# Optimization experiments

Measured on AMD Instinct MI355X. Metric: run time of the kernel, lower is better.

Reference implementation:

```python
import jax, jax.numpy as jnp
import numpy as np
from jax import lax

INF = jnp.float32(1e30)  # large finite stand-in for np.inf (keeps vjp NaN-free)


def setup_inputs() -> dict:
    key = jax.random.key(0)
    k1, k2 = jax.random.split(key)
    M = 2048
    N = 2048
    source = jax.random.normal(k1, (M,), dtype=jnp.float32)
    target = jax.random.normal(k2, (N,), dtype=jnp.float32)
    return {"source": source, "target": target}


def _dtw_sq(source, target):
    # DP over rows: row i holds DTW[i, 0..n]. Only two rows live at a time.
    n = target.shape[0]
    row0 = jnp.concatenate([jnp.zeros((1,), jnp.float32),
                            jnp.full((n,), INF, jnp.float32)])  # DTW[0, :]

    def row_step(prev_row, s_i):
        dists = (s_i - target) ** 2  # [n], cost of cell (i, j)

        def cell(left, xs):
            d, up_left, up = xs  # DTW[i-1,j-1], DTW[i-1,j]; left = DTW[i,j-1]
            cur = d + jnp.minimum(jnp.minimum(up, left), up_left)
            return cur, cur

        _, row_vals = lax.scan(cell, INF, (dists, prev_row[:-1], prev_row[1:]))
        new_row = jnp.concatenate([jnp.full((1,), INF, jnp.float32), row_vals])
        return new_row, None

    final_row, _ = lax.scan(row_step, row0, source)
    return final_row[-1]  # DTW[m, n]


def reference(source, target):
    loss_sq = _dtw_sq(source, target)
    return jnp.sqrt(loss_sq)[None]  # shape (1,), matching torch.Tensor([..])
```

## Files before the change

kernel.cpp:

```cpp
#include <hip/hip_runtime.h>
#include <math.h>


#define MM 2048
#define NN 2048
#define BR 8
#define BC 8
#define NT 256
#define NB (MM / BR)
#define NPH (NB + NT - 1)
#define EXW 9
#define SW 9
#define INFV 1e30f

__launch_bounds__(NT, 1)
__global__ void dtw_kernel(const float* __restrict__ src,
                           const float* __restrict__ tgt,
                           float* __restrict__ out)
{
    __shared__ float s_pad[NB * SW];
    __shared__ float ex[2][NT * EXW];

    const int tid = threadIdx.x;

    for (int i = tid; i < MM; i += NT)
        s_pad[(i >> 3) * SW + (i & 7)] = src[i];

    float tg[BC];
    #pragma unroll
    for (int k = 0; k < BC; ++k) tg[k] = tgt[tid * BC + k];

    float cur[BC];
    #pragma unroll
    for (int k = 0; k < BC; ++k) cur[k] = INFV;

    float corner = (tid == 0) ? 0.0f : INFV;

    __syncthreads();

    for (int p = 0; p < NPH; ++p) {
        const int bi = p - tid;
        if (0 <= bi && bi < NB) {
            float lc[BR];
            if (tid > 0) {
                const float* e = &ex[(p + 1) & 1][(tid - 1) * EXW];
                #pragma unroll
                for (int r = 0; r < BR; ++r) lc[r] = e[r];
            } else {
                #pragma unroll
                for (int r = 0; r < BR; ++r) lc[r] = INFV;
            }
            const float* sp = &s_pad[bi * SW];
            float srow[BR];
            #pragma unroll
            for (int r = 0; r < BR; ++r) srow[r] = sp[r];

            float rc[BR];
            float dl = corner;
            #pragma unroll
            for (int r = 0; r < BR; ++r) {
                float l  = lc[r];
                float sv = srow[r];
                float dgk = dl;
                #pragma unroll
                for (int k = 0; k < BC; ++k) {
                    float up = cur[k];
                    float m  = fminf(fminf(up, l), dgk);
                    float d  = sv - tg[k];
                    float v  = fmaf(d, d, m);
                    dgk = up;
                    cur[k] = v;
                    l = v;
                }
                rc[r] = l;
                dl = lc[r];
            }
            corner = lc[BR - 1];

            float* w = &ex[p & 1][tid * EXW];
            #pragma unroll
            for (int r = 0; r < BR; ++r) w[r] = rc[r];
        }
        __syncthreads();
    }

    if (tid == NT - 1)
        out[0] = sqrtf(cur[BC - 1]);
}

extern "C" void kernel_launch(void* const* d_in, const int* in_sizes, int n_in,
                              void* d_out, int out_size, void* d_ws, size_t ws_size,
                              hipStream_t stream)
{
    (void)in_sizes; (void)n_in; (void)out_size; (void)d_ws; (void)ws_size;
    const float* source = (const float*)d_in[0];
    const float* target = (const float*)d_in[1];
    float* out = (float*)d_out;
    dtw_kernel<<<1, NT, 0, stream>>>(source, target, out);
}
```

Measured before the change: 280.6 us.

## Pass DTW boundaries via wavefront shuffles and skewed mailboxes, sync every KK steps

Replaces the per-diagonal block-wide barrier and shared-memory boundary exchange with intra-wavefront __shfl_up for neighbour column values. Cross-wavefront boundaries go through a ring-buffer mailbox, and each wave is skewed by DELTA steps so it only needs a __syncthreads every KK iterations. The row tile drops to 4 and the cell updates are reordered into an anti-diagonal sweep to expose ILP. The cost is extra pipeline fill/drain from the skew and a total iteration count that grows to NB plus the maximum skew.

```diff
diff --git a/kernel.cpp b/kernel.cpp
--- a/kernel.cpp
+++ b/kernel.cpp
@@ -4,13 +4,16 @@
 
 #define MM 2048
 #define NN 2048
-#define BR 8
+#define BR 4
 #define BC 8
 #define NT 256
 #define NB (MM / BR)
-#define NPH (NB + NT - 1)
-#define EXW 9
-#define SW 9
+#define KK 16
+#define DELTA (63 + KK)
+#define MAXSKEW (63 + 3 * DELTA)
+#define NITER (NB + MAXSKEW)
+#define NSP ((NITER + KK - 1) / KK)
+#define RING (2 * KK)
 #define INFV 1e30f
 
 __launch_bounds__(NT, 1)
@@ -18,13 +21,16 @@
                            const float* __restrict__ tgt,
                            float* __restrict__ out)
 {
-    __shared__ float s_pad[NB * SW];
-    __shared__ float ex[2][NT * EXW];
+    __shared__ float4 s_src4[NB];
+    __shared__ float4 mbox[3][RING];
 
-    const int tid = threadIdx.x;
+    const int tid  = threadIdx.x;
+    const int wv   = tid >> 6;
+    const int ln   = tid & 63;
+    const int skew = ln + wv * DELTA;
 
-    for (int i = tid; i < MM; i += NT)
-        s_pad[(i >> 3) * SW + (i & 7)] = src[i];
+    const float4* s4 = (const float4*)src;
+    for (int i = tid; i < NB; i += NT) s_src4[i] = s4[i];
 
     float tg[BC];
     #pragma unroll
@@ -35,57 +41,67 @@
     for (int k = 0; k < BC; ++k) cur[k] = INFV;
 
     float corner = (tid == 0) ? 0.0f : INFV;
+    float4 rcp = make_float4(INFV, INFV, INFV, INFV);
 
     __syncthreads();
 
-    for (int p = 0; p < NPH; ++p) {
-        const int bi = p - tid;
-        if (0 <= bi && bi < NB) {
-            float lc[BR];
-            if (tid > 0) {
-                const float* e = &ex[(p + 1) & 1][(tid - 1) * EXW];
+    for (int sp = 0; sp < NSP; ++sp) {
+        #pragma unroll 1
+        for (int it = 0; it < KK; ++it) {
+            const int n = sp * KK + it;
+
+            float lc0 = __shfl_up(rcp.x, 1);
+            float lc1 = __shfl_up(rcp.y, 1);
+            float lc2 = __shfl_up(rcp.z, 1);
+            float lc3 = __shfl_up(rcp.w, 1);
+            if (ln == 0) {
+                if (wv == 0) {
+                    lc0 = lc1 = lc2 = lc3 = INFV;
+                } else {
+                    float4 m = mbox[wv - 1][(n - KK) & (RING - 1)];
+                    lc0 = m.x; lc1 = m.y; lc2 = m.z; lc3 = m.w;
+                }
+            }
+
+            const int bi = n - skew;
+            if (0 <= bi && bi < NB) {
+                float4 sv = s_src4[bi];
+                float srow[BR] = {sv.x, sv.y, sv.z, sv.w};
+                float lcx[BR]  = {lc0, lc1, lc2, lc3};
+
+                float dg[BR], lv[BR];
+                dg[0] = corner;
+                lv[0] = lcx[0];
                 #pragma unroll
-                for (int r = 0; r < BR; ++r) lc[r] = e[r];
-            } else {
+                for (int r = 1; r < BR; ++r) { dg[r] = lcx[r - 1]; lv[r] = lcx[r]; }
+
                 #pragma unroll
-                for (int r = 0; r < BR; ++r) lc[r] = INFV;
+                for (int s = 0; s < BR + BC - 1; ++s) {
+                    #pragma unroll
+                    for (int r = 0; r < BR; ++r) {
+                        const int k = s - r;
+                        if (0 <= k && k < BC) {
+                            float up = cur[k];
+                            float m  = fminf(fminf(up, lv[r]), dg[r]);
+                            float d  = srow[r] - tg[k];
+                            float v  = fmaf(d, d, m);
+                            dg[r] = up;
+                            lv[r] = v;
+                            cur[k] = v;
+                        }
+                    }
+                }
+
+                corner = lcx[BR - 1];
+                rcp = make_float4(lv[0], lv[1], lv[2], lv[3]);
+                if (ln == 63 && wv < 3)
+                    mbox[wv][n & (RING - 1)] = rcp;
             }
-            const float* sp = &s_pad[bi * SW];
-            float srow[BR];
-            #pragma unroll
-            for (int r = 0; r < BR; ++r) srow[r] = sp[r];
-
-            float rc[BR];
-            float dl = corner;
-            #pragma unroll
-            for (int r = 0; r < BR; ++r) {
-                float l  = lc[r];
-                float sv = srow[r];
-                float dgk = dl;
-                #pragma unroll
-                for (int k = 0; k < BC; ++k) {
-                    float up = cur[k];
-                    float m  = fminf(fminf(up, l), dgk);
-                    float d  = sv - tg[k];
-                    float v  = fmaf(d, d, m);
-                    dgk = up;
-                    cur[k] = v;
-                    l = v;
-                }
-                rc[r] = l;
-                dl = lc[r];
-            }
-            corner = lc[BR - 1];
-
-            float* w = &ex[p & 1][tid * EXW];
-            #pragma unroll
-            for (int r = 0; r < BR; ++r) w[r] = rc[r];
         }
         __syncthreads();
     }
 
-    if (tid == NT - 1)
-        out[0] = sqrtf(cur[BC - 1]);
+    if (tid == NT - 1) out[0] = sqrtf(cur[BC - 1]);
 }
 
 extern "C" void kernel_launch(void* const* d_in, const int* in_sizes, int n_in,
```

Result: faster. 262.8 us (-6.3%).
